# Optimization experiments

Measured on AMD Instinct MI355X. Metric: run time of the kernel, lower is better.

## Reference

```python
import jax, jax.numpy as jnp
import numpy as np

N_NODES = 50000
N_EDGES = 640000
N_REL = 8
IN_DIM = 128
HID_DIM = 128
OUT_DIM = 64


def setup_inputs() -> dict:
    key = jax.random.key(0)
    ks = jax.random.split(key, 8)
    features = jax.random.normal(ks[0], (N_NODES, IN_DIM), dtype=jnp.float32)
    src = jax.random.randint(ks[1], (N_EDGES,), 0, N_NODES, dtype=jnp.int32)
    dst = jax.random.randint(ks[2], (N_EDGES,), 0, N_NODES, dtype=jnp.int32)
    edge_types = jax.random.randint(ks[3], (N_EDGES,), 0, N_REL, dtype=jnp.int32)
    s1 = 1.0 / np.sqrt(IN_DIM)
    s2 = 1.0 / np.sqrt(HID_DIM)
    W1 = jax.random.normal(ks[4], (N_REL, IN_DIM, HID_DIM), dtype=jnp.float32) * s1
    W1_self = jax.random.normal(ks[5], (IN_DIM, HID_DIM), dtype=jnp.float32) * s1
    b1 = jnp.zeros((HID_DIM,), dtype=jnp.float32)
    W2 = jax.random.normal(ks[6], (N_REL, HID_DIM, OUT_DIM), dtype=jnp.float32) * s2
    W2_self = jax.random.normal(ks[7], (HID_DIM, OUT_DIM), dtype=jnp.float32) * s2
    b2 = jnp.zeros((OUT_DIM,), dtype=jnp.float32)
    return {"features": features, "src": src, "dst": dst, "edge_types": edge_types,
            "W1": W1, "W1_self": W1_self, "b1": b1,
            "W2": W2, "W2_self": W2_self, "b2": b2}


def _rel_graph_conv(h, src, dst, edge_types, W, W_self, b):
    # Precompute relation-specific transforms for all nodes: [R, N, Dout]
    rel = jnp.einsum('nd,rdo->rno', h, W)
    # Gather per-edge message W[etype(e)] @ h[src(e)]: [E, Dout]
    msg = rel[edge_types, src]
    # Scatter-sum to destination nodes
    agg = jax.ops.segment_sum(msg, dst, num_segments=h.shape[0])
    # Self-loop + bias (DGL RelGraphConv defaults: self_loop=True, bias=True)
    return agg + h @ W_self + b


def reference(features, src, dst, edge_types, W1, W1_self, b1, W2, W2_self, b2):
    h = jax.nn.relu(_rel_graph_conv(features, src, dst, edge_types, W1, W1_self, b1))
    logits = _rel_graph_conv(h, src, dst, edge_types, W2, W2_self, b2)
    return logits
```

## Files before the change

### kernel.cpp

```cpp
#include <hip/hip_runtime.h>
#include <hip/hip_bf16.h>
#include <stdint.h>

#define NN 50000
#define NE 640000
#define NR 8
#define NK (NR * NN)
#define NB2 ((NK + 1023) / 1024)

typedef short bf16x8 __attribute__((ext_vector_type(8)));
typedef float f32x4  __attribute__((ext_vector_type(4)));

__device__ __forceinline__ unsigned short f2bf(float f) {
    union { float f; unsigned u; } v; v.f = f;
    unsigned r = v.u + 0x7FFF + ((v.u >> 16) & 1);
    return (unsigned short)(r >> 16);
}

__global__ void hist2_kernel(const int* __restrict__ dst, const int* __restrict__ et,
                             int* __restrict__ counts) {
    int e = blockIdx.x * 256 + threadIdx.x;
    if (e < NE) atomicAdd(&counts[et[e] * NN + dst[e]], 1);
}

__global__ __launch_bounds__(1024) void blocksum_kernel(const int* __restrict__ counts,
                                                        int* __restrict__ bsum, int n) {
    __shared__ int ws[16];
    int i = blockIdx.x * 1024 + threadIdx.x;
    int v = (i < n) ? counts[i] : 0;
    #pragma unroll
    for (int d = 32; d > 0; d >>= 1) v += __shfl_down(v, d, 64);
    int wid = threadIdx.x >> 6, lane = threadIdx.x & 63;
    if (lane == 0) ws[wid] = v;
    __syncthreads();
    if (threadIdx.x < 16) {
        int s = ws[threadIdx.x];
        #pragma unroll
        for (int d = 8; d > 0; d >>= 1) s += __shfl_down(s, d, 16);
        if (threadIdx.x == 0) bsum[blockIdx.x] = s;
    }
}

__global__ __launch_bounds__(512) void scanbase_kernel(const int* __restrict__ bsum,
                                                       int* __restrict__ base,
                                                       int* __restrict__ total, int nb) {
    __shared__ int ws[8];
    int t = threadIdx.x, lane = t & 63, wid = t >> 6;
    int v = (t < nb) ? bsum[t] : 0;
    int incl = v;
    #pragma unroll
    for (int d = 1; d < 64; d <<= 1) {
        int nv = __shfl_up(incl, d, 64);
        if (lane >= d) incl += nv;
    }
    if (lane == 63) ws[wid] = incl;
    __syncthreads();
    if (t < 8) {
        int s = ws[t], si = s;
        #pragma unroll
        for (int d = 1; d < 8; d <<= 1) {
            int nv = __shfl_up(si, d, 64);
            if (t >= d) si += nv;
        }
        ws[t] = si - s;
    }
    __syncthreads();
    int excl = ws[wid] + incl - v;
    if (t < nb) base[t] = excl;
    if (t == 511) total[0] = ws[7] + incl;
}

__global__ __launch_bounds__(1024) void scanlocal_kernel(const int* __restrict__ counts,
                                                         const int* __restrict__ base,
                                                         int* __restrict__ offsets,
                                                         int* __restrict__ cursor, int n) {
    __shared__ int ws[16];
    __shared__ int wbase[16];
    int t = threadIdx.x;
    int i = blockIdx.x * 1024 + t;
    int v = (i < n) ? counts[i] : 0;
    int lane = t & 63, wid = t >> 6;
    int incl = v;
    #pragma unroll
    for (int d = 1; d < 64; d <<= 1) {
        int nv = __shfl_up(incl, d, 64);
        if (lane >= d) incl += nv;
    }
    if (lane == 63) ws[wid] = incl;
    __syncthreads();
    if (t < 16) {
        int s = ws[t], si = s;
        #pragma unroll
        for (int d = 1; d < 16; d <<= 1) {
            int nv = __shfl_up(si, d, 16);
            if (t >= d) si += nv;
        }
        wbase[t] = si - s;
    }
    __syncthreads();
    if (i < n) {
        int excl = base[blockIdx.x] + wbase[wid] + incl - v;
        offsets[i] = excl;
        cursor[i]  = excl;
    }
}

__global__ void fill2_kernel(const int* __restrict__ src, const int* __restrict__ dst,
                             const int* __restrict__ et, int* __restrict__ cursor,
                             int* __restrict__ esrc) {
    int e = blockIdx.x * 256 + threadIdx.x;
    if (e < NE) {
        int pos = atomicAdd(&cursor[et[e] * NN + dst[e]], 1);
        esrc[pos] = src[e];
    }
}

__global__ void cvt_bf16_kernel(const float* __restrict__ in, unsigned short* __restrict__ outp,
                                int n8) {
    int i = blockIdx.x * 256 + threadIdx.x;
    if (i >= n8) return;
    const float4* pp = (const float4*)in + (size_t)i * 2;
    float4 a = pp[0], b = pp[1];
    uint4 o;
    o.x = (unsigned)f2bf(a.x) | ((unsigned)f2bf(a.y) << 16);
    o.y = (unsigned)f2bf(a.z) | ((unsigned)f2bf(a.w) << 16);
    o.z = (unsigned)f2bf(b.x) | ((unsigned)f2bf(b.y) << 16);
    o.w = (unsigned)f2bf(b.z) | ((unsigned)f2bf(b.w) << 16);
    ((uint4*)outp)[i] = o;
}

template<int DOUTV>
__global__ void prepW_kernel(const float* __restrict__ W, const float* __restrict__ Wself,
                             unsigned short* __restrict__ WT) {
    int idx = blockIdx.x * 256 + threadIdx.x;
    if (idx >= 9 * DOUTV * 128) return;
    int k = idx & 127;
    int c = idx >> 7;
    int r = c / DOUTV;
    int o = c - r * DOUTV;
    float v = (r < 8) ? W[((size_t)r * 128 + k) * DOUTV + o]
                      : Wself[(size_t)k * DOUTV + o];
    WT[idx] = f2bf(v);
}

template<int NOUT, bool RELU, bool OUTBF16>
__global__ __launch_bounds__(256) void fused_layer(
        const unsigned short* __restrict__ A,
        const unsigned short* __restrict__ WT,
        const float* __restrict__ bias,
        const int* __restrict__ off2,
        const int* __restrict__ esrc,
        void* __restrict__ outp, int M) {
    constexpr int CW = NOUT / 4;
    constexpr int NJ = CW / 16;
    __shared__ unsigned short Asw[64 * 128];

    const int t = threadIdx.x;
    const int n0 = blockIdx.x * 64;
    const int bm = (M - n0 < 64) ? (M - n0) : 64;
    const int lane = t & 63;
    const int w = t >> 6;
    const int r15 = lane & 15;
    const int q = lane >> 4;

    const int key = t >> 2;
    const int sub = t & 3;
    const int kk = n0 + key;
    const bool kv = (kk < M);

    f32x4 acc[4][NJ] = {};

    auto do_mfma = [&](int rr) {
        #pragma unroll
        for (int ks = 0; ks < 4; ks++) {
            int c = (ks * 4 + q) ^ r15;
            bf16x8 af[4];
            #pragma unroll
            for (int i = 0; i < 4; i++)
                af[i] = *(const bf16x8*)((const char*)Asw + (i * 16 + r15) * 256 + (c << 4));
            #pragma unroll
            for (int j = 0; j < NJ; j++) {
                bf16x8 bf = *(const bf16x8*)(WT +
                    ((size_t)(rr * NOUT + w * CW + j * 16 + r15) << 7) + ks * 32 + q * 8);
                #pragma unroll
                for (int i = 0; i < 4; i++)
                    acc[i][j] = __builtin_amdgcn_mfma_f32_16x16x32_bf16(af[i], bf, acc[i][j], 0, 0, 0);
            }
        }
    };

    int e0 = kv ? off2[kk] : 0;
    int e1 = kv ? off2[kk + 1] : 0;

    #pragma unroll
    for (int kc = 0; kc < 4; kc++) {
        int g = t + kc * 256;
        int row = g >> 4, c = g & 15;
        uint4 v = make_uint4(0, 0, 0, 0);
        if (row < bm) v = *(const uint4*)(A + ((size_t)(n0 + row) << 7) + c * 8);
        *(uint4*)((char*)Asw + row * 256 + ((c ^ (row & 15)) << 4)) = v;
    }
    __syncthreads();
    do_mfma(8);

    for (int r = 0; r < 8; r++) {
        int e0n = 0, e1n = 0;
        if (r < 7 && kv) {
            e0n = off2[(r + 1) * NN + kk];
            e1n = off2[(r + 1) * NN + kk + 1];
        }

        float a[32];
        #pragma unroll
        for (int i = 0; i < 32; i++) a[i] = 0.f;
        for (int e = e0; e < e1; ++e) {
            int s = esrc[e];
            const uint4* rp = (const uint4*)((const unsigned*)A + ((size_t)s << 6) + sub * 16);
            #pragma unroll
            for (int u4 = 0; u4 < 4; ++u4) {
                uint4 v = rp[u4];
                unsigned uu[4] = {v.x, v.y, v.z, v.w};
                #pragma unroll
                for (int j = 0; j < 4; ++j) {
                    a[u4 * 8 + j * 2 + 0] += __uint_as_float(uu[j] << 16);
                    a[u4 * 8 + j * 2 + 1] += __uint_as_float(uu[j] & 0xffff0000u);
                }
            }
        }
        __syncthreads();

        #pragma unroll
        for (int c4 = 0; c4 < 4; ++c4) {
            uint4 pv;
            pv.x = (unsigned)f2bf(a[c4 * 8 + 0]) | ((unsigned)f2bf(a[c4 * 8 + 1]) << 16);
            pv.y = (unsigned)f2bf(a[c4 * 8 + 2]) | ((unsigned)f2bf(a[c4 * 8 + 3]) << 16);
            pv.z = (unsigned)f2bf(a[c4 * 8 + 4]) | ((unsigned)f2bf(a[c4 * 8 + 5]) << 16);
            pv.w = (unsigned)f2bf(a[c4 * 8 + 6]) | ((unsigned)f2bf(a[c4 * 8 + 7]) << 16);
            int c = sub * 4 + c4;
            *(uint4*)((char*)Asw + key * 256 + ((c ^ (key & 15)) << 4)) = pv;
        }
        __syncthreads();

        do_mfma(r);
        e0 = e0n; e1 = e1n;
    }

    #pragma unroll
    for (int j = 0; j < NJ; j++) {
        int col = w * CW + j * 16 + r15;
        float bv = bias[col];
        #pragma unroll
        for (int i = 0; i < 4; i++) {
            #pragma unroll
            for (int reg = 0; reg < 4; reg++) {
                int m = n0 + i * 16 + q * 4 + reg;
                if (m < M) {
                    float v = acc[i][j][reg] + bv;
                    if (RELU) v = fmaxf(v, 0.f);
                    if (OUTBF16)
                        ((unsigned short*)outp)[(size_t)m * NOUT + col] = f2bf(v);
                    else
                        ((float*)outp)[(size_t)m * NOUT + col] = v;
                }
            }
        }
    }
}

extern "C" void kernel_launch(void* const* d_in, const int* in_sizes, int n_in,
                              void* d_out, int out_size, void* d_ws, size_t ws_size,
                              hipStream_t stream) {
    const float* X   = (const float*)d_in[0];
    const int*   src = (const int*)d_in[1];
    const int*   dst = (const int*)d_in[2];
    const int*   et  = (const int*)d_in[3];
    const float* W1  = (const float*)d_in[4];
    const float* W1s = (const float*)d_in[5];
    const float* b1  = (const float*)d_in[6];
    const float* W2  = (const float*)d_in[7];
    const float* W2s = (const float*)d_in[8];
    const float* b2  = (const float*)d_in[9];
    float* out = (float*)d_out;

    char* p = (char*)d_ws;
    unsigned short* Xbf = (unsigned short*)p; p += (size_t)NN * 128 * 2;
    unsigned short* hbf = (unsigned short*)p; p += (size_t)NN * 128 * 2;
    unsigned short* W1T = (unsigned short*)p; p += (size_t)9 * 128 * 128 * 2;
    unsigned short* W2T = (unsigned short*)p; p += (size_t)9 * 64 * 128 * 2;
    int* counts2 = (int*)p; p += (size_t)NK * 4;
    int* off2    = (int*)p; p += (size_t)(NK + 4) * 4;
    int* cursor2 = (int*)p; p += (size_t)NK * 4;
    int* esrc    = (int*)p; p += (size_t)NE * 4;
    int* bsum    = (int*)p; p += 512 * 4;
    int* bbase   = (int*)p; p += 512 * 4;

    hipMemsetAsync(counts2, 0, (size_t)NK * sizeof(int), stream);
    hist2_kernel<<<(NE + 255) / 256, 256, 0, stream>>>(dst, et, counts2);
    blocksum_kernel<<<NB2, 1024, 0, stream>>>(counts2, bsum, NK);
    scanbase_kernel<<<1, 512, 0, stream>>>(bsum, bbase, &off2[NK], NB2);
    scanlocal_kernel<<<NB2, 1024, 0, stream>>>(counts2, bbase, off2, cursor2, NK);
    fill2_kernel<<<(NE + 255) / 256, 256, 0, stream>>>(src, dst, et, cursor2, esrc);

    cvt_bf16_kernel<<<(NN * 128 / 8 + 255) / 256, 256, 0, stream>>>(X, Xbf, NN * 128 / 8);
    prepW_kernel<128><<<(9 * 128 * 128 + 255) / 256, 256, 0, stream>>>(W1, W1s, W1T);
    prepW_kernel<64><<<(9 * 64 * 128 + 255) / 256, 256, 0, stream>>>(W2, W2s, W2T);

    const int nblk = (NN + 63) / 64;

    fused_layer<128, true, true><<<nblk, 256, 0, stream>>>(
        Xbf, W1T, b1, off2, esrc, hbf, NN);
    fused_layer<64, false, false><<<nblk, 256, 0, stream>>>(
        hbf, W2T, b2, off2, esrc, out, NN);
}
```

Baseline: 301.7 us.

## Halve node tile, double-buffer LDS, and unroll edge gather by two

Cuts the per-block node tile from 64 to 32 rows, so each node row is gathered by 8 threads (16 features each) instead of 4. This doubles the number of blocks and shortens each thread's serial edge loop. The edge loop now processes two edges per iteration, using a zero-weight FMA as a tail guard, to put more independent loads in flight. It also double-buffers the shared A tile between relations. The cost is that each block's weight tiles are reloaded for half as many rows, which doubles weight traffic per node.

```diff
diff --git a/kernel.cpp b/kernel.cpp
--- a/kernel.cpp
+++ b/kernel.cpp
@@ -151,39 +151,40 @@
         const int* __restrict__ off2,
         const int* __restrict__ esrc,
         void* __restrict__ outp, int M) {
+    constexpr int BM = 32;
     constexpr int CW = NOUT / 4;
     constexpr int NJ = CW / 16;
-    __shared__ unsigned short Asw[64 * 128];
+    __shared__ unsigned short Asw[2][BM * 128];
 
     const int t = threadIdx.x;
-    const int n0 = blockIdx.x * 64;
-    const int bm = (M - n0 < 64) ? (M - n0) : 64;
+    const int n0 = blockIdx.x * BM;
+    const int bm = (M - n0 < BM) ? (M - n0) : BM;
     const int lane = t & 63;
     const int w = t >> 6;
     const int r15 = lane & 15;
     const int q = lane >> 4;
 
-    const int key = t >> 2;
-    const int sub = t & 3;
-    const int kk = n0 + key;
+    const int trow = t >> 3;
+    const int sub  = t & 7;
+    const int kk = n0 + trow;
     const bool kv = (kk < M);
 
-    f32x4 acc[4][NJ] = {};
-
-    auto do_mfma = [&](int rr) {
+    f32x4 acc[2][NJ] = {};
+
+    auto do_mfma = [&](int b, int rr) {
         #pragma unroll
         for (int ks = 0; ks < 4; ks++) {
             int c = (ks * 4 + q) ^ r15;
-            bf16x8 af[4];
+            bf16x8 af[2];
             #pragma unroll
-            for (int i = 0; i < 4; i++)
-                af[i] = *(const bf16x8*)((const char*)Asw + (i * 16 + r15) * 256 + (c << 4));
+            for (int i = 0; i < 2; i++)
+                af[i] = *(const bf16x8*)((const char*)Asw[b] + (i * 16 + r15) * 256 + (c << 4));
             #pragma unroll
             for (int j = 0; j < NJ; j++) {
                 bf16x8 bf = *(const bf16x8*)(WT +
                     ((size_t)(rr * NOUT + w * CW + j * 16 + r15) << 7) + ks * 32 + q * 8);
                 #pragma unroll
-                for (int i = 0; i < 4; i++)
+                for (int i = 0; i < 2; i++)
                     acc[i][j] = __builtin_amdgcn_mfma_f32_16x16x32_bf16(af[i], bf, acc[i][j], 0, 0, 0);
             }
         }
@@ -193,15 +194,15 @@
     int e1 = kv ? off2[kk + 1] : 0;
 
     #pragma unroll
-    for (int kc = 0; kc < 4; kc++) {
+    for (int kc = 0; kc < 2; kc++) {
         int g = t + kc * 256;
         int row = g >> 4, c = g & 15;
         uint4 v = make_uint4(0, 0, 0, 0);
         if (row < bm) v = *(const uint4*)(A + ((size_t)(n0 + row) << 7) + c * 8);
-        *(uint4*)((char*)Asw + row * 256 + ((c ^ (row & 15)) << 4)) = v;
-    }
-    __syncthreads();
-    do_mfma(8);
+        *(uint4*)((char*)Asw[0] + row * 256 + ((c ^ (row & 15)) << 4)) = v;
+    }
+    __syncthreads();
+    do_mfma(0, 8);
 
     for (int r = 0; r < 8; r++) {
         int e0n = 0, e1n = 0;
@@ -210,38 +211,46 @@
             e1n = off2[(r + 1) * NN + kk + 1];
         }
 
-        float a[32];
-        #pragma unroll
-        for (int i = 0; i < 32; i++) a[i] = 0.f;
-        for (int e = e0; e < e1; ++e) {
-            int s = esrc[e];
-            const uint4* rp = (const uint4*)((const unsigned*)A + ((size_t)s << 6) + sub * 16);
+        float a[16];
+        #pragma unroll
+        for (int i = 0; i < 16; i++) a[i] = 0.f;
+
+        auto accum = [&](uint4 v, int base, float wt) {
+            unsigned uu[4] = {v.x, v.y, v.z, v.w};
             #pragma unroll
-            for (int u4 = 0; u4 < 4; ++u4) {
-                uint4 v = rp[u4];
-                unsigned uu[4] = {v.x, v.y, v.z, v.w};
-                #pragma unroll
-                for (int j = 0; j < 4; ++j) {
-                    a[u4 * 8 + j * 2 + 0] += __uint_as_float(uu[j] << 16);
-                    a[u4 * 8 + j * 2 + 1] += __uint_as_float(uu[j] & 0xffff0000u);
-                }
+            for (int j = 0; j < 4; j++) {
+                a[base + j * 2 + 0] = fmaf(wt, __uint_as_float(uu[j] << 16), a[base + j * 2 + 0]);
+                a[base + j * 2 + 1] = fmaf(wt, __uint_as_float(uu[j] & 0xffff0000u), a[base + j * 2 + 1]);
             }
+        };
+
+        for (int e = e0; e < e1; e += 2) {
+            int s0 = esrc[e];
+            int s1 = esrc[(e + 1 < e1) ? e + 1 : e];
+            float w1 = (e + 1 < e1) ? 1.f : 0.f;
+            const uint4* rp0 = (const uint4*)((const unsigned*)A + ((size_t)s0 << 6) + sub * 8);
+            const uint4* rp1 = (const uint4*)((const unsigned*)A + ((size_t)s1 << 6) + sub * 8);
+            uint4 va0 = rp0[0], vb0 = rp0[1];
+            uint4 va1 = rp1[0], vb1 = rp1[1];
+            accum(va0, 0, 1.f); accum(vb0, 8, 1.f);
+            accum(va1, 0, w1);  accum(vb1, 8, w1);
         }
         __syncthreads();
 
-        #pragma unroll
-        for (int c4 = 0; c4 < 4; ++c4) {
+        int b = (r + 1) & 1;
+        #pragma unroll
+        for (int c4 = 0; c4 < 2; ++c4) {
             uint4 pv;
             pv.x = (unsigned)f2bf(a[c4 * 8 + 0]) | ((unsigned)f2bf(a[c4 * 8 + 1]) << 16);
             pv.y = (unsigned)f2bf(a[c4 * 8 + 2]) | ((unsigned)f2bf(a[c4 * 8 + 3]) << 16);
             pv.z = (unsigned)f2bf(a[c4 * 8 + 4]) | ((unsigned)f2bf(a[c4 * 8 + 5]) << 16);
             pv.w = (unsigned)f2bf(a[c4 * 8 + 6]) | ((unsigned)f2bf(a[c4 * 8 + 7]) << 16);
-            int c = sub * 4 + c4;
-            *(uint4*)((char*)Asw + key * 256 + ((c ^ (key & 15)) << 4)) = pv;
+            int c = sub * 2 + c4;
+            *(uint4*)((char*)Asw[b] + trow * 256 + ((c ^ (trow & 15)) << 4)) = pv;
         }
         __syncthreads();
 
-        do_mfma(r);
+        do_mfma(b, r);
         e0 = e0n; e1 = e1n;
     }
 
@@ -250,7 +259,7 @@
         int col = w * CW + j * 16 + r15;
         float bv = bias[col];
         #pragma unroll
-        for (int i = 0; i < 4; i++) {
+        for (int i = 0; i < 2; i++) {
             #pragma unroll
             for (int reg = 0; reg < 4; reg++) {
                 int m = n0 + i * 16 + q * 4 + reg;
@@ -305,7 +314,7 @@
     prepW_kernel<128><<<(9 * 128 * 128 + 255) / 256, 256, 0, stream>>>(W1, W1s, W1T);
     prepW_kernel<64><<<(9 * 64 * 128 + 255) / 256, 256, 0, stream>>>(W2, W2s, W2T);
 
-    const int nblk = (NN + 63) / 64;
+    const int nblk = (NN + 31) / 32;
 
     fused_layer<128, true, true><<<nblk, 256, 0, stream>>>(
         Xbf, W1T, b1, off2, esrc, hbf, NN);
```

Result: slower. 334.4 us (+10.8%).

## Split fused gather-GEMM into separate wave-per-segment aggregation and LDS-tiled GEMM kernels

Applied to the files above, without the earlier changes.

The fused per-layer kernel, which gathered neighbor rows for each relation inside the GEMM block, is replaced by two kernels. The first is a wave-per-(relation,node) aggregation kernel that writes per-relation sums to a large bf16 workspace. The second is a GEMM kernel that stages both the A tiles and the weight tiles in LDS and writes coalesced output through shared memory. This aims to give the irregular gather its own parallelism and memory-level parallelism. In exchange it adds a round trip through an ~100MB intermediate buffer (8×50000×128 bf16) for each layer, plus extra kernel launches.

```diff
diff --git a/kernel.cpp b/kernel.cpp
--- a/kernel.cpp
+++ b/kernel.cpp
@@ -143,126 +143,148 @@
     WT[idx] = f2bf(v);
 }
 
+__global__ __launch_bounds__(256) void agg_seg(
+        const unsigned short* __restrict__ A,
+        const int* __restrict__ off2,
+        const int* __restrict__ esrc,
+        unsigned short* __restrict__ agg) {
+    int wv = threadIdx.x >> 6, l = threadIdx.x & 63;
+    int k = blockIdx.x * 4 + wv;
+    int e0 = off2[k], e1 = off2[k + 1];
+    const unsigned* R = (const unsigned*)A;
+    float ax = 0.f, ay = 0.f;
+    int j = e0;
+    for (; j + 4 <= e1; j += 4) {
+        int s0 = esrc[j], s1 = esrc[j + 1], s2 = esrc[j + 2], s3 = esrc[j + 3];
+        unsigned p0 = R[((size_t)s0 << 6) + l];
+        unsigned p1 = R[((size_t)s1 << 6) + l];
+        unsigned p2 = R[((size_t)s2 << 6) + l];
+        unsigned p3 = R[((size_t)s3 << 6) + l];
+        ax += __uint_as_float(p0 << 16) + __uint_as_float(p1 << 16)
+            + __uint_as_float(p2 << 16) + __uint_as_float(p3 << 16);
+        ay += __uint_as_float(p0 & 0xffff0000u) + __uint_as_float(p1 & 0xffff0000u)
+            + __uint_as_float(p2 & 0xffff0000u) + __uint_as_float(p3 & 0xffff0000u);
+    }
+    for (; j < e1; ++j) {
+        unsigned p = R[((size_t)esrc[j] << 6) + l];
+        ax += __uint_as_float(p << 16);
+        ay += __uint_as_float(p & 0xffff0000u);
+    }
+    ((unsigned*)agg)[((size_t)k << 6) + l] = (unsigned)f2bf(ax) | ((unsigned)f2bf(ay) << 16);
+}
+
 template<int NOUT, bool RELU, bool OUTBF16>
-__global__ __launch_bounds__(256) void fused_layer(
-        const unsigned short* __restrict__ A,
+__global__ __launch_bounds__(256) void gemm_sum(
+        const unsigned short* __restrict__ agg,
+        const unsigned short* __restrict__ feat,
         const unsigned short* __restrict__ WT,
         const float* __restrict__ bias,
-        const int* __restrict__ off2,
-        const int* __restrict__ esrc,
         void* __restrict__ outp, int M) {
-    constexpr int CW = NOUT / 4;
-    constexpr int NJ = CW / 16;
-    __shared__ unsigned short Asw[64 * 128];
+    constexpr int NJ = NOUT / 32;
+    __shared__ __align__(16) unsigned char smem[16384 + NOUT * 256];
+    unsigned short* As = (unsigned short*)smem;
+    unsigned short* Ws = (unsigned short*)(smem + 16384);
 
     const int t = threadIdx.x;
     const int n0 = blockIdx.x * 64;
-    const int bm = (M - n0 < 64) ? (M - n0) : 64;
     const int lane = t & 63;
     const int w = t >> 6;
     const int r15 = lane & 15;
     const int q = lane >> 4;
-
-    const int key = t >> 2;
-    const int sub = t & 3;
-    const int kk = n0 + key;
-    const bool kv = (kk < M);
-
-    f32x4 acc[4][NJ] = {};
-
-    auto do_mfma = [&](int rr) {
+    const int wm = (w & 1) * 32;
+    const int wn = (w >> 1) * (NOUT / 2);
+
+    f32x4 acc[2][NJ] = {};
+
+    for (int r = 0; r < 9; ++r) {
+        const unsigned short* Ab = (r < 8) ? agg + (((size_t)r * NN) << 7) : feat;
+        __syncthreads();
+        #pragma unroll
+        for (int i = 0; i < 4; i++) {
+            int g = t + i * 256;
+            int row = g >> 4, c = g & 15;
+            int m = n0 + row;
+            uint4 v = make_uint4(0, 0, 0, 0);
+            if (m < M) v = *(const uint4*)(Ab + ((size_t)m << 7) + c * 8);
+            *(uint4*)((char*)As + row * 256 + ((c ^ (row & 15)) << 4)) = v;
+        }
+        #pragma unroll
+        for (int i = 0; i < NOUT / 16; i++) {
+            int g = t + i * 256;
+            int row = g >> 4, c = g & 15;
+            uint4 v = *(const uint4*)(WT + ((size_t)(r * NOUT + row) << 7) + c * 8);
+            *(uint4*)((char*)Ws + row * 256 + ((c ^ (row & 15)) << 4)) = v;
+        }
+        __syncthreads();
         #pragma unroll
         for (int ks = 0; ks < 4; ks++) {
             int c = (ks * 4 + q) ^ r15;
-            bf16x8 af[4];
+            bf16x8 af[2];
             #pragma unroll
-            for (int i = 0; i < 4; i++)
-                af[i] = *(const bf16x8*)((const char*)Asw + (i * 16 + r15) * 256 + (c << 4));
+            for (int i = 0; i < 2; i++)
+                af[i] = *(const bf16x8*)((const char*)As + (wm + i * 16 + r15) * 256 + (c << 4));
             #pragma unroll
             for (int j = 0; j < NJ; j++) {
-                bf16x8 bf = *(const bf16x8*)(WT +
-                    ((size_t)(rr * NOUT + w * CW + j * 16 + r15) << 7) + ks * 32 + q * 8);
+                bf16x8 bf = *(const bf16x8*)((const char*)Ws + (wn + j * 16 + r15) * 256 + (c << 4));
                 #pragma unroll
-                for (int i = 0; i < 4; i++)
+                for (int i = 0; i < 2; i++)
                     acc[i][j] = __builtin_amdgcn_mfma_f32_16x16x32_bf16(af[i], bf, acc[i][j], 0, 0, 0);
             }
         }
-    };
-
-    int e0 = kv ? off2[kk] : 0;
-    int e1 = kv ? off2[kk + 1] : 0;
-
-    #pragma unroll
-    for (int kc = 0; kc < 4; kc++) {
-        int g = t + kc * 256;
-        int row = g >> 4, c = g & 15;
-        uint4 v = make_uint4(0, 0, 0, 0);
-        if (row < bm) v = *(const uint4*)(A + ((size_t)(n0 + row) << 7) + c * 8);
-        *(uint4*)((char*)Asw + row * 256 + ((c ^ (row & 15)) << 4)) = v;
-    }
-    __syncthreads();
-    do_mfma(8);
-
-    for (int r = 0; r < 8; r++) {
-        int e0n = 0, e1n = 0;
-        if (r < 7 && kv) {
-            e0n = off2[(r + 1) * NN + kk];
-            e1n = off2[(r + 1) * NN + kk + 1];
-        }
-
-        float a[32];
-        #pragma unroll
-        for (int i = 0; i < 32; i++) a[i] = 0.f;
-        for (int e = e0; e < e1; ++e) {
-            int s = esrc[e];
-            const uint4* rp = (const uint4*)((const unsigned*)A + ((size_t)s << 6) + sub * 16);
+    }
+    __syncthreads();
+
+    if (OUTBF16) {
+        unsigned short* Cs = (unsigned short*)smem;
+        #pragma unroll
+        for (int j = 0; j < NJ; j++) {
+            int n = wn + j * 16 + r15;
+            float bv = bias[n];
             #pragma unroll
-            for (int u4 = 0; u4 < 4; ++u4) {
-                uint4 v = rp[u4];
-                unsigned uu[4] = {v.x, v.y, v.z, v.w};
+            for (int i = 0; i < 2; i++) {
                 #pragma unroll
-                for (int j = 0; j < 4; ++j) {
-                    a[u4 * 8 + j * 2 + 0] += __uint_as_float(uu[j] << 16);
-                    a[u4 * 8 + j * 2 + 1] += __uint_as_float(uu[j] & 0xffff0000u);
+                for (int reg = 0; reg < 4; reg++) {
+                    float v = acc[i][j][reg] + bv;
+                    if (RELU) v = fmaxf(v, 0.f);
+                    Cs[(wm + i * 16 + q * 4 + reg) * 136 + n] = f2bf(v);
                 }
             }
         }
         __syncthreads();
-
-        #pragma unroll
-        for (int c4 = 0; c4 < 4; ++c4) {
-            uint4 pv;
-            pv.x = (unsigned)f2bf(a[c4 * 8 + 0]) | ((unsigned)f2bf(a[c4 * 8 + 1]) << 16);
-            pv.y = (unsigned)f2bf(a[c4 * 8 + 2]) | ((unsigned)f2bf(a[c4 * 8 + 3]) << 16);
-            pv.z = (unsigned)f2bf(a[c4 * 8 + 4]) | ((unsigned)f2bf(a[c4 * 8 + 5]) << 16);
-            pv.w = (unsigned)f2bf(a[c4 * 8 + 6]) | ((unsigned)f2bf(a[c4 * 8 + 7]) << 16);
-            int c = sub * 4 + c4;
-            *(uint4*)((char*)Asw + key * 256 + ((c ^ (key & 15)) << 4)) = pv;
-        }
-        __syncthreads();
-
-        do_mfma(r);
-        e0 = e0n; e1 = e1n;
-    }
-
-    #pragma unroll
-    for (int j = 0; j < NJ; j++) {
-        int col = w * CW + j * 16 + r15;
-        float bv = bias[col];
-        #pragma unroll
-        for (int i = 0; i < 4; i++) {
+        unsigned short* O = (unsigned short*)outp;
+        #pragma unroll
+        for (int i = 0; i < (NOUT == 128 ? 4 : 2); i++) {
+            int g = t + i * 256;
+            int row = g / (NOUT / 8), c = g % (NOUT / 8);
+            int m = n0 + row;
+            if (m < M)
+                *(uint4*)(O + (size_t)m * NOUT + c * 8) = *(const uint4*)(Cs + row * 136 + c * 8);
+        }
+    } else {
+        float* Cs = (float*)smem;
+        #pragma unroll
+        for (int j = 0; j < NJ; j++) {
+            int n = wn + j * 16 + r15;
+            float bv = bias[n];
             #pragma unroll
-            for (int reg = 0; reg < 4; reg++) {
-                int m = n0 + i * 16 + q * 4 + reg;
-                if (m < M) {
+            for (int i = 0; i < 2; i++) {
+                #pragma unroll
+                for (int reg = 0; reg < 4; reg++) {
                     float v = acc[i][j][reg] + bv;
                     if (RELU) v = fmaxf(v, 0.f);
-                    if (OUTBF16)
-                        ((unsigned short*)outp)[(size_t)m * NOUT + col] = f2bf(v);
-                    else
-                        ((float*)outp)[(size_t)m * NOUT + col] = v;
+                    Cs[(wm + i * 16 + q * 4 + reg) * 68 + n] = v;
                 }
             }
+        }
+        __syncthreads();
+        float* O = (float*)outp;
+        #pragma unroll
+        for (int i = 0; i < NOUT / 16; i++) {
+            int g = t + i * 256;
+            int row = g / (NOUT / 4), c = g % (NOUT / 4);
+            int m = n0 + row;
+            if (m < M)
+                *(uint4*)(O + (size_t)m * NOUT + c * 4) = *(const uint4*)(Cs + row * 68 + c * 4);
         }
     }
 }
@@ -283,6 +305,7 @@
     float* out = (float*)d_out;
 
     char* p = (char*)d_ws;
+    unsigned short* agg = (unsigned short*)p; p += (size_t)NK * 128 * 2;
     unsigned short* Xbf = (unsigned short*)p; p += (size_t)NN * 128 * 2;
     unsigned short* hbf = (unsigned short*)p; p += (size_t)NN * 128 * 2;
     unsigned short* W1T = (unsigned short*)p; p += (size_t)9 * 128 * 128 * 2;
@@ -305,10 +328,11 @@
     prepW_kernel<128><<<(9 * 128 * 128 + 255) / 256, 256, 0, stream>>>(W1, W1s, W1T);
     prepW_kernel<64><<<(9 * 64 * 128 + 255) / 256, 256, 0, stream>>>(W2, W2s, W2T);
 
-    const int nblk = (NN + 63) / 64;
-
-    fused_layer<128, true, true><<<nblk, 256, 0, stream>>>(
-        Xbf, W1T, b1, off2, esrc, hbf, NN);
-    fused_layer<64, false, false><<<nblk, 256, 0, stream>>>(
-        hbf, W2T, b2, off2, esrc, out, NN);
-}
+    const int gblk = (NN + 63) / 64;
+
+    agg_seg<<<NK / 4, 256, 0, stream>>>(Xbf, off2, esrc, agg);
+    gemm_sum<128, true, true><<<gblk, 256, 0, stream>>>(agg, Xbf, W1T, b1, hbf, NN);
+
+    agg_seg<<<NK / 4, 256, 0, stream>>>(hbf, off2, esrc, agg);
+    gemm_sum<64, false, false><<<gblk, 256, 0, stream>>>(agg, hbf, W2T, b2, out, NN);
+}
```

After: 438.9 us. 1.45x slower.
